# Kernel tuning notes

Measured on AMD Instinct MI355X. Metric: run time of the kernel, lower is better.

## Reference

```python
import jax, jax.numpy as jnp
import numpy as np

B, LAGS, POOL, D, H, NTS = 16, 4096, 4, 512, 8, 1000
S = LAGS // POOL          # num_pools = 1024
DH = D // H               # head dim = 64


def _layernorm_dim1(x, gamma, beta, eps=1e-5):
    # torch code: mean/var over dim=1 (channel axis), unbiased var, per-position affine
    mean = jnp.mean(x, axis=1, keepdims=True)
    var = jnp.var(x, axis=1, keepdims=True, ddof=1)
    unit = (x - mean) / jnp.sqrt(eps + var)
    return gamma * unit + beta


def setup_inputs() -> dict:
    key = jax.random.key(0)
    ks = jax.random.split(key, 16)
    inp = {
        "ts": jax.random.normal(ks[0], (B, 1, LAGS), dtype=jnp.float32),
        "te": jax.random.randint(ks[1], (B, 1), 0, NTS),
        "conv_w": jax.random.normal(ks[2], (D, 1, POOL), dtype=jnp.float32) * (1.0 / POOL) ** 0.5,
        "conv_b": jax.random.normal(ks[3], (D,), dtype=jnp.float32) * 0.02,
        "pe_emb": jax.random.normal(ks[4], (S, D), dtype=jnp.float32),
        "ts_emb": jax.random.normal(ks[5], (NTS, D), dtype=jnp.float32),
        "ln1_g": jnp.ones((S,), dtype=jnp.float32),
        "ln1_b": jnp.zeros((S,), dtype=jnp.float32),
        "dense_M": jax.random.normal(ks[6], (D, D), dtype=jnp.float32) * D ** -0.5,
        "Wq": jax.random.normal(ks[7], (H, DH, D), dtype=jnp.float32) * D ** -0.5,
        "Wk": jax.random.normal(ks[8], (H, DH, D), dtype=jnp.float32) * D ** -0.5,
        "Wv": jax.random.normal(ks[9], (H, DH, D), dtype=jnp.float32) * D ** -0.5,
        "Wo": jax.random.normal(ks[10], (D, D), dtype=jnp.float32) * D ** -0.5,
        "bo": jnp.zeros((D, 1), dtype=jnp.float32),
        "ln2_g": jnp.ones((S,), dtype=jnp.float32),
        "ln2_b": jnp.zeros((S,), dtype=jnp.float32),
    }
    return inp


def _forward(ts, te, conv_w, conv_b, pe_emb, ts_emb, ln1_g, ln1_b,
             dense_M, Wq, Wk, Wv, Wo, bo, ln2_g, ln2_b):
    # Conv1d with stride == kernel_size: non-overlapping patches
    xr = ts.reshape(B, S, POOL)                                   # (B,S,P)
    conv = jnp.einsum('bsp,dp->bds', xr, conv_w[:, 0, :]) + conv_b[:, None]  # (B,D,S)
    conv = conv + pe_emb.T                                        # positional add (D,S)
    act = jax.nn.gelu(conv, approximate=False)
    n1 = _layernorm_dim1(act, ln1_g, ln1_b)
    dense = jnp.einsum('ed,bds->bes', dense_M, n1)                # Linear: M @ x
    dense = dense + ts_emb[te[:, 0]][:, :, None]                  # ts embedding (B,D,1)

    # multi-head attention, Q=K=V=dense; vectorized over heads
    Qd = jnp.einsum('hcd,bds->bhcs', Wq, dense)                   # (B,H,DH,S)
    Kd = jnp.einsum('hcd,bds->bhcs', Wk, dense)
    Vd = jnp.einsum('hcd,bds->bhcs', Wv, dense)
    scores = jnp.einsum('bhci,bhcj->bhij', Qd, Kd) / DH ** 0.5    # (B,H,S,S)
    i_idx = jnp.arange(S)
    mask = i_idx[:, None] > i_idx[None, :]                        # tril(diagonal=-1): i>j -> -inf
    scores = jnp.where(mask, -jnp.inf, scores)
    sm = jax.nn.softmax(scores, axis=2)                           # softmax over dim 1 of (S,S)
    attn = jnp.einsum('bhci,bhij->bhcj', Vd, sm)                  # V @ softmaxed
    cat = attn.reshape(B, D, S)                                   # concat heads on dim 1
    out = jnp.einsum('ed,bds->bes', Wo, cat) + bo[None]           # final linear + bias
    res = out + conv                                              # residual
    return _layernorm_dim1(res, ln2_g, ln2_b)


def reference(ts, te, conv_w, conv_b, pe_emb, ts_emb, ln1_g, ln1_b,
              dense_M, Wq, Wk, Wv, Wo, bo, ln2_g, ln2_b):
    return _forward(ts, te, conv_w, conv_b, pe_emb, ts_emb, ln1_g, ln1_b,
                    dense_M, Wq, Wk, Wv, Wo, bo, ln2_g, ln2_b)
```

## Files before the change

### kernel.cpp

```cpp
#include <hip/hip_runtime.h>
#include <hip/hip_bf16.h>

#define B_ 16
#define S_ 1024
#define D_ 512
#define H_ 8
#define DH_ 64

typedef __attribute__((ext_vector_type(8))) short bf16x8;
typedef __attribute__((ext_vector_type(4))) short bf16x4;
typedef __attribute__((ext_vector_type(4))) float f32x4;
typedef __attribute__((ext_vector_type(16))) float f32x16;

__device__ __forceinline__ short f2bf(float f) {
    __hip_bfloat16 h = __float2bfloat16(f);
    return *reinterpret_cast<short*>(&h);
}
__device__ __forceinline__ unsigned pack_bf2(float lo, float hi) {
    unsigned a = (unsigned)(unsigned short)f2bf(lo);
    unsigned b = (unsigned)(unsigned short)f2bf(hi);
    return a | (b << 16);
}
__device__ __forceinline__ void gload16(const void* g, void* l) {
    __builtin_amdgcn_global_load_lds(
        (const __attribute__((address_space(1))) unsigned int*)g,
        (__attribute__((address_space(3))) unsigned int*)l, 16, 0, 0);
}

__global__ __launch_bounds__(256) void prep_w(
    const float* __restrict__ M, const float* __restrict__ Wq,
    const float* __restrict__ Wk, const float* __restrict__ Wv,
    const float* __restrict__ Wo, __hip_bfloat16* __restrict__ wb)
{
    __hip_bfloat16* wsrc = wb;
    __hip_bfloat16* Wob  = wb + 786432;
    __hip_bfloat16* MT   = wb + 1048576;

    const int gid = blockIdx.x * 256 + threadIdx.x;
    const int e8 = gid * 8;
    const int w = e8 >> 18;
    const int off = e8 & 262143;
    const float* src = (w == 0) ? M : (w == 1) ? Wq : (w == 2) ? Wk
                      : (w == 3) ? Wv : Wo;
    const float scale = (w == 1) ? 0.18033688011112042f : 1.0f;
    const float4 f0 = *reinterpret_cast<const float4*>(src + off);
    const float4 f1 = *reinterpret_cast<const float4*>(src + off + 4);
    float fv[8] = {f0.x, f0.y, f0.z, f0.w, f1.x, f1.y, f1.z, f1.w};

    if (w == 0) {
        const int e = off >> 9, d0 = off & 511;
#pragma unroll
        for (int j = 0; j < 8; ++j)
            MT[(size_t)(d0 + j) * 512 + e] = __float2bfloat16(fv[j]);
    } else {
        union { short s[8]; bf16x8 v; } r;
#pragma unroll
        for (int j = 0; j < 8; ++j) r.s[j] = f2bf(fv[j] * scale);
        __hip_bfloat16* dst = (w == 4) ? (Wob + off) : (wsrc + (w - 1) * 262144 + off);
        *reinterpret_cast<bf16x8*>(dst) = r.v;
    }
}

__global__ __launch_bounds__(256) void bias_k(
    const float* __restrict__ Wq, const float* __restrict__ Wk,
    const float* __restrict__ Wv, const float* __restrict__ ts_emb,
    const int* __restrict__ te, float* __restrict__ qkvbias)
{
    const int blk = blockIdx.x;
    const int w = blk >> 4, b = blk & 15;
    const float* W = (w == 0) ? Wq : (w == 1) ? Wk : Wv;
    const float scale = (w == 0) ? 0.18033688011112042f : 1.0f;
    const float* e = ts_emb + (size_t)te[b] * 512;
#pragma unroll
    for (int rep = 0; rep < 2; ++rep) {
        const int n = threadIdx.x + rep * 256;
        const float* wr = W + (size_t)n * 512;
        float s = 0.f;
        for (int d = 0; d < 512; d += 4) {
            const float4 a = *reinterpret_cast<const float4*>(wr + d);
            const float4 bb = *reinterpret_cast<const float4*>(e + d);
            s += a.x * bb.x + a.y * bb.y + a.z * bb.z + a.w * bb.w;
        }
        qkvbias[(size_t)(w * 16 + b) * 512 + n] = s * scale;
    }
}

__global__ __launch_bounds__(256) void k1_conv_gelu_ln(
    const float* __restrict__ ts, const float* __restrict__ conv_w,
    const float* __restrict__ conv_b, const float* __restrict__ pe,
    const float* __restrict__ g1, const float* __restrict__ b1,
    __hip_bfloat16* __restrict__ n1)
{
    const int w = threadIdx.x >> 6, lane = threadIdx.x & 63;
    const int row = blockIdx.x * 4 + w;
    const int b = row >> 10, s = row & 1023;
    const float4 x = *reinterpret_cast<const float4*>(ts + b * 4096 + s * 4);
    const int d0 = lane * 8;

    const float4 cb0 = *reinterpret_cast<const float4*>(conv_b + d0);
    const float4 cb1 = *reinterpret_cast<const float4*>(conv_b + d0 + 4);
    const float4 pe0 = *reinterpret_cast<const float4*>(pe + s * 512 + d0);
    const float4 pe1 = *reinterpret_cast<const float4*>(pe + s * 512 + d0 + 4);
    const float cbv[8] = {cb0.x, cb0.y, cb0.z, cb0.w, cb1.x, cb1.y, cb1.z, cb1.w};
    const float pev[8] = {pe0.x, pe0.y, pe0.z, pe0.w, pe1.x, pe1.y, pe1.z, pe1.w};

    float a[8];
    float sum = 0.f, sq = 0.f;
#pragma unroll
    for (int j = 0; j < 8; ++j) {
        const float4 wv = *reinterpret_cast<const float4*>(conv_w + (d0 + j) * 4);
        float v = x.x * wv.x + x.y * wv.y + x.z * wv.z + x.w * wv.w
                + cbv[j] + pev[j];
        v = 0.5f * v * (1.0f + erff(v * 0.70710678118654752f));
        a[j] = v; sum += v; sq += v * v;
    }
#pragma unroll
    for (int off = 1; off < 64; off <<= 1) {
        sum += __shfl_xor(sum, off);
        sq  += __shfl_xor(sq, off);
    }
    const float mean = sum * (1.0f / 512.0f);
    const float var  = (sq - 512.0f * mean * mean) * (1.0f / 511.0f);
    const float rstd = rsqrtf(var + 1e-5f);
    const float gg = g1[s], bb = b1[s];
    union { short sh[8]; bf16x8 v; } o;
#pragma unroll
    for (int j = 0; j < 8; ++j)
        o.sh[j] = f2bf(gg * ((a[j] - mean) * rstd) + bb);
    *reinterpret_cast<bf16x8*>(n1 + (size_t)row * 512 + d0) = o.v;
}

template<int MODE>
__global__ __launch_bounds__(256, 2) void gemm_k(
    const __hip_bfloat16* __restrict__ A,
    const __hip_bfloat16* __restrict__ Wb,
    void* __restrict__ outp,
    const float* __restrict__ aux)
{
    __shared__ char lA[2][128 * 128];
    __shared__ char lB[2][128 * 128];

    const int t = threadIdx.x;
    const int lane = t & 63;
    const int w = t >> 6;
    const int wm = w & 1, wn = w >> 1;
    const int Rb = blockIdx.x * 128;
    const int Nb = blockIdx.y * 128;
    const int g = lane >> 4, lr = lane & 15;
    const int lrow = lane >> 3;
    const int coff = ((lane & 7) ^ lrow) * 8;

    const __hip_bfloat16* asrc = A  + (size_t)(Rb + lrow) * 512 + coff;
    const __hip_bfloat16* bsrc = Wb + (size_t)(Nb + lrow) * 512 + coff;

    f32x4 acc[4][4];
#pragma unroll
    for (int i = 0; i < 4; ++i)
#pragma unroll
        for (int j = 0; j < 4; ++j) acc[i][j] = {0.f, 0.f, 0.f, 0.f};

    auto stage = [&](int buf, int k0) {
#pragma unroll
        for (int i = 0; i < 4; ++i) {
            const int r0 = w * 32 + i * 8;
            gload16(asrc + (size_t)r0 * 512 + k0, &lA[buf][r0 * 128]);
        }
#pragma unroll
        for (int i = 0; i < 4; ++i) {
            const int r0 = w * 32 + i * 8;
            gload16(bsrc + (size_t)r0 * 512 + k0, &lB[buf][r0 * 128]);
        }
    };

    stage(0, 0);
    __syncthreads();

    for (int kt = 0; kt < 8; ++kt) {
        const int buf = kt & 1;
        if (kt < 7) stage(buf ^ 1, (kt + 1) * 64);
#pragma unroll
        for (int kk = 0; kk < 2; ++kk) {
            bf16x8 af[4], bfv[4];
            const int ch = kk * 4 + g;
#pragma unroll
            for (int mt = 0; mt < 4; ++mt) {
                const int row = wm * 64 + mt * 16 + lr;
                af[mt] = *reinterpret_cast<const bf16x8*>(
                    &lA[buf][row * 128 + ((ch ^ (row & 7)) << 4)]);
            }
#pragma unroll
            for (int nt = 0; nt < 4; ++nt) {
                const int row = wn * 64 + nt * 16 + lr;
                bfv[nt] = *reinterpret_cast<const bf16x8*>(
                    &lB[buf][row * 128 + ((ch ^ (row & 7)) << 4)]);
            }
#pragma unroll
            for (int mt = 0; mt < 4; ++mt)
#pragma unroll
                for (int nt = 0; nt < 4; ++nt)
                    acc[mt][nt] = __builtin_amdgcn_mfma_f32_16x16x32_bf16(
                        af[mt], bfv[nt], acc[mt][nt], 0, 0, 0);
        }
        __syncthreads();
    }

    const int w3 = Nb >> 9;
#pragma unroll
    for (int mt = 0; mt < 4; ++mt) {
#pragma unroll
        for (int nt = 0; nt < 4; ++nt) {
#pragma unroll
            for (int r = 0; r < 4; ++r) {
                const int R = Rb + wm * 64 + mt * 16 + 4 * g + r;
                const int N = Nb + wn * 64 + nt * 16 + lr;
                float v = acc[mt][nt][r];
                if (MODE == 5) {
                    const int Nl = N & 511;
                    const int b = R >> 10, s = R & 1023, h = Nl >> 6, c = Nl & 63;
                    v += aux[(size_t)(w3 * 16 + b) * 512 + Nl];
                    __hip_bfloat16* base =
                        reinterpret_cast<__hip_bfloat16*>(outp) + (size_t)w3 * 8388608;
                    if (w3 == 2)
                        base[(((size_t)(b * 8 + h)) * 64 + c) * 1024 + s] =
                            __float2bfloat16(v);
                    else
                        base[(((size_t)(b * 8 + h)) * 1024 + s) * 64 + c] =
                            __float2bfloat16(v);
                } else if (MODE == 6) {
                    reinterpret_cast<__hip_bfloat16*>(outp)[(size_t)R * 512 + N] =
                        __float2bfloat16(v);
                } else {
                    reinterpret_cast<float*>(outp)[(size_t)R * 512 + N] = v + aux[N];
                }
            }
        }
    }
}

__device__ __forceinline__ void write_strip(
    __hip_bfloat16* __restrict__ dstbase, const int jw0,
    const f32x16& o0, const f32x16& o1, const float lsum,
    const int l5, const int ln31)
{
    const float linv = 1.0f / lsum;
#pragma unroll
    for (int r = 0; r < 16; ++r) {
        const int jrow = (r & 3) + 8 * (r >> 2) + 4 * l5;
        const float rinv = __shfl(linv, jrow);
        __hip_bfloat16* dst = dstbase + (size_t)(jw0 + jrow) * 512;
        dst[ln31]      = __float2bfloat16(o0[r] * rinv);
        dst[32 + ln31] = __float2bfloat16(o1[r] * rinv);
    }
}

__global__ __launch_bounds__(256, 4) void attn5_k(
    const __hip_bfloat16* __restrict__ Qm,
    const __hip_bfloat16* __restrict__ Km,
    const __hip_bfloat16* __restrict__ Vt,
    __hip_bfloat16* __restrict__ cat)
{
    __shared__ char qbuf[2][4096];
    __shared__ char vbuf[2][4096];

    const int t = threadIdx.x, lane = t & 63, w = t >> 6;
    const int l5 = lane >> 5, ln31 = lane & 31;
    const int id = blockIdx.x;
    const int bh = id & 127;
    const int jb = (0x32451067u >> ((id >> 7) * 4)) & 7;
    const int b = bh >> 3, h = bh & 7;
    const int j0 = jb * 128 + w * 32;

    const __hip_bfloat16* Qh = Qm + (size_t)bh * (S_ * 64);
    const __hip_bfloat16* Kh = Km + (size_t)bh * (S_ * 64);
    const __hip_bfloat16* Vh = Vt + (size_t)bh * (64 * S_);

    bf16x8 kf[4];
#pragma unroll
    for (int kt = 0; kt < 4; ++kt)
        kf[kt] = *reinterpret_cast<const bf16x8*>(
            Kh + (size_t)(j0 + ln31) * 64 + kt * 16 + l5 * 8);

    f32x16 o0, o1;
#pragma unroll
    for (int r = 0; r < 16; ++r) { o0[r] = 0.f; o1[r] = 0.f; }
    float m = -3e38f, lsum = 0.f;

    const int last = jb * 4 + w;
    const int ntiles = jb * 4 + 4;

    const int q_row  = w * 8 + (lane >> 3);
    const int q_ch   = (lane & 7) ^ (lane >> 3);
    const int v_row  = w * 16 + (lane >> 2);
    const int v_ch   = (lane & 3) ^ ((lane >> 2) & 3) ^ ((lane >> 4) & 3);
    const __hip_bfloat16* qsrc = Qh + (size_t)q_row * 64 + q_ch * 8;
    const __hip_bfloat16* vsrc = Vh + (size_t)v_row * 1024 + v_ch * 8;

    auto stage = [&](int buf, int tile) {
        const int i0 = tile * 32;
        gload16(qsrc + (size_t)i0 * 64, &qbuf[buf][w * 1024]);
        gload16(vsrc + i0,              &vbuf[buf][w * 1024]);
    };

    stage(0, 0);
    __syncthreads();

    for (int tt = 0; tt < ntiles; ++tt) {
        const int buf = tt & 1;
        if (tt + 1 < ntiles) stage(buf ^ 1, tt + 1);
        if (tt <= last) {
            f32x16 sc;
#pragma unroll
            for (int r = 0; r < 16; ++r) sc[r] = 0.f;
            bf16x8 qf[4];
#pragma unroll
            for (int kt = 0; kt < 4; ++kt)
                qf[kt] = *reinterpret_cast<const bf16x8*>(
                    &qbuf[buf][ln31 * 128 + (((kt * 2 + l5) ^ (ln31 & 7)) << 4)]);
#pragma unroll
            for (int kt = 0; kt < 4; ++kt)
                sc = __builtin_amdgcn_mfma_f32_32x32x16_bf16(qf[kt], kf[kt], sc, 0, 0, 0);

            union u8 { bf16x4 h[2]; bf16x8 v; };
            u8 vf[2][2];
#pragma unroll
            for (int kt = 0; kt < 2; ++kt) {
#pragma unroll
                for (int dh = 0; dh < 2; ++dh) {
                    const int drow = ln31 + dh * 32;
                    const int swz = (drow & 3) ^ ((drow >> 2) & 3);
                    const int x0 = kt * 32 + 8 * l5;
#pragma unroll
                    for (int hp = 0; hp < 2; ++hp) {
                        const int x = x0 + hp * 16;
                        vf[kt][dh].h[hp] = *reinterpret_cast<const bf16x4*>(
                            &vbuf[buf][drow * 64 + (((x >> 4) ^ swz) << 4) + (x & 15)]);
                    }
                }
            }

            const bool diag = (tt == last);
            float p[16];
            float mx = -3e38f;
            if (diag) {
#pragma unroll
                for (int r = 0; r < 16; ++r) {
                    const int irow = (r & 3) + 8 * (r >> 2) + 4 * l5;
                    const float v = (irow > ln31) ? -3e38f : sc[r];
                    p[r] = v; mx = fmaxf(mx, v);
                }
            } else {
#pragma unroll
                for (int r = 0; r < 16; ++r) { p[r] = sc[r]; mx = fmaxf(mx, sc[r]); }
            }
            mx = fmaxf(mx, __shfl_xor(mx, 32));
            if (!__all(mx <= m + 8.0f)) {
                const float mn = fmaxf(m, mx);
                const float alpha = exp2f(m - mn);
                m = mn; lsum *= alpha;
#pragma unroll
                for (int r = 0; r < 16; ++r) {
                    const int jrow = (r & 3) + 8 * (r >> 2) + 4 * l5;
                    const float ar = __shfl(alpha, jrow);
                    o0[r] *= ar; o1[r] *= ar;
                }
            }
            float ps = 0.f;
#pragma unroll
            for (int r = 0; r < 16; ++r) { p[r] = exp2f(p[r] - m); ps += p[r]; }
            ps += __shfl_xor(ps, 32);
            lsum += ps;

            union { unsigned u[4]; bf16x8 v; } pa0, pa1;
            pa0.u[0] = pack_bf2(p[0],  p[1]);  pa0.u[1] = pack_bf2(p[2],  p[3]);
            pa0.u[2] = pack_bf2(p[4],  p[5]);  pa0.u[3] = pack_bf2(p[6],  p[7]);
            pa1.u[0] = pack_bf2(p[8],  p[9]);  pa1.u[1] = pack_bf2(p[10], p[11]);
            pa1.u[2] = pack_bf2(p[12], p[13]); pa1.u[3] = pack_bf2(p[14], p[15]);
            o0 = __builtin_amdgcn_mfma_f32_32x32x16_bf16(pa0.v, vf[0][0].v, o0, 0, 0, 0);
            o1 = __builtin_amdgcn_mfma_f32_32x32x16_bf16(pa0.v, vf[0][1].v, o1, 0, 0, 0);
            o0 = __builtin_amdgcn_mfma_f32_32x32x16_bf16(pa1.v, vf[1][0].v, o0, 0, 0, 0);
            o1 = __builtin_amdgcn_mfma_f32_32x32x16_bf16(pa1.v, vf[1][1].v, o1, 0, 0, 0);
        }
        __syncthreads();
    }

    __hip_bfloat16* dstbase = cat + (size_t)b * 1024 * 512 + h * 64;
    write_strip(dstbase, j0, o0, o1, lsum, l5, ln31);
}

__global__ __launch_bounds__(256) void k5_res_ln(
    const float* __restrict__ outf,
    const float* __restrict__ ts, const float* __restrict__ conv_w,
    const float* __restrict__ conv_b, const float* __restrict__ pe,
    const float* __restrict__ g2, const float* __restrict__ b2,
    float* __restrict__ out)
{
    __shared__ float tile[16 * 520];
    const int blk = blockIdx.x;
    const int b = blk >> 6, s0 = (blk & 63) * 16;
    const int t = threadIdx.x;
    const int sl = t >> 4, c = t & 15;
    const int s = s0 + sl;

    const float4 x = *reinterpret_cast<const float4*>(ts + b * 4096 + s * 4);
    float vals[32];
    float sum = 0.f, sq = 0.f;
#pragma unroll
    for (int j = 0; j < 32; ++j) {
        const int d = c + 16 * j;
        const float4 wv = *reinterpret_cast<const float4*>(conv_w + d * 4);
        const float conv = x.x * wv.x + x.y * wv.y + x.z * wv.z + x.w * wv.w
                         + conv_b[d] + pe[s * 512 + d];
        const float a = outf[(size_t)(b * 1024 + s) * 512 + d] + conv;
        vals[j] = a; sum += a; sq += a * a;
    }
#pragma unroll
    for (int off = 1; off < 16; off <<= 1) {
        sum += __shfl_xor(sum, off);
        sq  += __shfl_xor(sq, off);
    }
    const float mean = sum * (1.0f / 512.0f);
    const float var  = (sq - 512.0f * mean * mean) * (1.0f / 511.0f);
    const float rstd = rsqrtf(var + 1e-5f);
    const float gg = g2[s], bb = b2[s];
#pragma unroll
    for (int j = 0; j < 32; ++j) {
        const int d = c + 16 * j;
        tile[sl * 520 + d] = gg * ((vals[j] - mean) * rstd) + bb;
    }
    __syncthreads();
#pragma unroll
    for (int q2 = 0; q2 < 2; ++q2) {
        const int d = t + q2 * 256;
        float buf[16];
#pragma unroll
        for (int sl2 = 0; sl2 < 16; ++sl2) buf[sl2] = tile[sl2 * 520 + d];
        float4* dst = reinterpret_cast<float4*>(
            out + ((size_t)b * 512 + d) * 1024 + s0);
        dst[0] = make_float4(buf[0],  buf[1],  buf[2],  buf[3]);
        dst[1] = make_float4(buf[4],  buf[5],  buf[6],  buf[7]);
        dst[2] = make_float4(buf[8],  buf[9],  buf[10], buf[11]);
        dst[3] = make_float4(buf[12], buf[13], buf[14], buf[15]);
    }
}

extern "C" void kernel_launch(void* const* d_in, const int* in_sizes, int n_in,
                              void* d_out, int out_size, void* d_ws, size_t ws_size,
                              hipStream_t stream)
{
    const float* ts     = (const float*)d_in[0];
    const int*   te     = (const int*)d_in[1];
    const float* conv_w = (const float*)d_in[2];
    const float* conv_b = (const float*)d_in[3];
    const float* pe     = (const float*)d_in[4];
    const float* ts_emb = (const float*)d_in[5];
    const float* g1     = (const float*)d_in[6];
    const float* b1     = (const float*)d_in[7];
    const float* M      = (const float*)d_in[8];
    const float* Wq     = (const float*)d_in[9];
    const float* Wk     = (const float*)d_in[10];
    const float* Wv     = (const float*)d_in[11];
    const float* Wo     = (const float*)d_in[12];
    const float* bo     = (const float*)d_in[13];
    const float* g2     = (const float*)d_in[14];
    const float* b2     = (const float*)d_in[15];

    char* ws = (char*)d_ws;
    __hip_bfloat16* wb     = (__hip_bfloat16*)(ws);
    __hip_bfloat16* wsrc   = wb;
    __hip_bfloat16* Wob    = wb + 786432;
    __hip_bfloat16* MT     = wb + 1048576;
    __hip_bfloat16* Wqkvp  = (__hip_bfloat16*)(ws + (2688ull << 10));
    float*          qkvbias= (float*)(ws + (4608ull << 10));
    __hip_bfloat16* n1     = (__hip_bfloat16*)(ws + ( 6ull << 20));
    __hip_bfloat16* cat    = n1;
    __hip_bfloat16* q      = (__hip_bfloat16*)(ws + (22ull << 20));
    __hip_bfloat16* k      = (__hip_bfloat16*)(ws + (38ull << 20));
    __hip_bfloat16* vT     = (__hip_bfloat16*)(ws + (54ull << 20));
    float*          outf   = (float*)(ws + (22ull << 20));

    prep_w<<<640, 256, 0, stream>>>(M, Wq, Wk, Wv, Wo, wb);
    bias_k<<<48, 256, 0, stream>>>(Wq, Wk, Wv, ts_emb, te, qkvbias);
    gemm_k<6><<<dim3(12, 4), 256, 0, stream>>>(wsrc, MT, Wqkvp, nullptr);
    k1_conv_gelu_ln<<<4096, 256, 0, stream>>>(ts, conv_w, conv_b, pe, g1, b1, n1);
    gemm_k<5><<<dim3(128, 12), 256, 0, stream>>>(n1, Wqkvp, q, qkvbias);
    attn5_k<<<1024, 256, 0, stream>>>(q, k, vT, cat);
    gemm_k<3><<<dim3(128, 4), 256, 0, stream>>>(cat, Wob, outf, bo);
    k5_res_ln<<<1024, 256, 0, stream>>>(outf, ts, conv_w, conv_b, pe, g2, b2,
                                        (float*)d_out);
}
```

Baseline: 198.1 us.

## Transpose M via LDS tiles and split bias dot products across blocks

prep_w now transposes the dense matrix through a 32x33 shared-memory tile, so the MT writes are coalesced instead of strided scalar stores. bias_k now reads the bf16 prescaled weights and splits each 512-long dot product into four 128-element chunks across 4x more blocks, writing partial sums. The QKV GEMM epilogue adds the four partials together. This raises parallelism in small prep kernels, at the cost of extra epilogue loads and of using bf16-rounded weights in the bias, which slightly changes precision.

```diff
diff --git a/kernel.cpp b/kernel.cpp
--- a/kernel.cpp
+++ b/kernel.cpp
@@ -16,6 +16,10 @@
     __hip_bfloat16 h = __float2bfloat16(f);
     return *reinterpret_cast<short*>(&h);
 }
+__device__ __forceinline__ float bf2f(short s) {
+    unsigned u = ((unsigned)(unsigned short)s) << 16;
+    return __uint_as_float(u);
+}
 __device__ __forceinline__ unsigned pack_bf2(float lo, float hi) {
     unsigned a = (unsigned)(unsigned short)f2bf(lo);
     unsigned b = (unsigned)(unsigned short)f2bf(hi);
@@ -36,52 +40,60 @@
     __hip_bfloat16* Wob  = wb + 786432;
     __hip_bfloat16* MT   = wb + 1048576;
 
-    const int gid = blockIdx.x * 256 + threadIdx.x;
-    const int e8 = gid * 8;
-    const int w = e8 >> 18;
-    const int off = e8 & 262143;
-    const float* src = (w == 0) ? M : (w == 1) ? Wq : (w == 2) ? Wk
-                      : (w == 3) ? Wv : Wo;
-    const float scale = (w == 1) ? 0.18033688011112042f : 1.0f;
-    const float4 f0 = *reinterpret_cast<const float4*>(src + off);
-    const float4 f1 = *reinterpret_cast<const float4*>(src + off + 4);
-    float fv[8] = {f0.x, f0.y, f0.z, f0.w, f1.x, f1.y, f1.z, f1.w};
-
-    if (w == 0) {
-        const int e = off >> 9, d0 = off & 511;
-#pragma unroll
-        for (int j = 0; j < 8; ++j)
-            MT[(size_t)(d0 + j) * 512 + e] = __float2bfloat16(fv[j]);
+    const int blk = blockIdx.x, t = threadIdx.x;
+    if (blk < 512) {
+        const int wi = blk >> 7;
+        const int off = (blk & 127) * 2048 + t * 8;
+        const float* src = (wi == 0) ? Wq : (wi == 1) ? Wk : (wi == 2) ? Wv : Wo;
+        const float scale = (wi == 0) ? 0.18033688011112042f : 1.0f;
+        const float4 f0 = *reinterpret_cast<const float4*>(src + off);
+        const float4 f1 = *reinterpret_cast<const float4*>(src + off + 4);
+        const float fv[8] = {f0.x, f0.y, f0.z, f0.w, f1.x, f1.y, f1.z, f1.w};
+        union { short s[8]; bf16x8 v; } r;
+#pragma unroll
+        for (int j = 0; j < 8; ++j) r.s[j] = f2bf(fv[j] * scale);
+        __hip_bfloat16* dst = (wi == 3) ? (Wob + off) : (wsrc + wi * 262144 + off);
+        *reinterpret_cast<bf16x8*>(dst) = r.v;
     } else {
-        union { short s[8]; bf16x8 v; } r;
-#pragma unroll
-        for (int j = 0; j < 8; ++j) r.s[j] = f2bf(fv[j] * scale);
-        __hip_bfloat16* dst = (w == 4) ? (Wob + off) : (wsrc + (w - 1) * 262144 + off);
-        *reinterpret_cast<bf16x8*>(dst) = r.v;
+        __shared__ float tile[32][33];
+        const int tt = blk - 512;
+        const int e0 = (tt & 15) * 32, d0 = (tt >> 4) * 32;
+        const int r = t >> 5, c = t & 31;
+#pragma unroll
+        for (int k = 0; k < 4; ++k)
+            tile[r + k * 8][c] = M[(size_t)(e0 + r + k * 8) * 512 + d0 + c];
+        __syncthreads();
+#pragma unroll
+        for (int k = 0; k < 4; ++k)
+            MT[(size_t)(d0 + r + k * 8) * 512 + e0 + c] =
+                __float2bfloat16(tile[c][r + k * 8]);
     }
 }
 
 __global__ __launch_bounds__(256) void bias_k(
-    const float* __restrict__ Wq, const float* __restrict__ Wk,
-    const float* __restrict__ Wv, const float* __restrict__ ts_emb,
-    const int* __restrict__ te, float* __restrict__ qkvbias)
+    const __hip_bfloat16* __restrict__ wsrc, const float* __restrict__ ts_emb,
+    const int* __restrict__ te, float* __restrict__ qkvpart)
 {
     const int blk = blockIdx.x;
-    const int w = blk >> 4, b = blk & 15;
-    const float* W = (w == 0) ? Wq : (w == 1) ? Wk : Wv;
-    const float scale = (w == 0) ? 0.18033688011112042f : 1.0f;
-    const float* e = ts_emb + (size_t)te[b] * 512;
+    const int w16b = blk >> 2, dc = blk & 3;
+    const int b = w16b & 15, w = w16b >> 4;
+    const float* e = ts_emb + (size_t)te[b] * 512 + dc * 128;
 #pragma unroll
     for (int rep = 0; rep < 2; ++rep) {
         const int n = threadIdx.x + rep * 256;
-        const float* wr = W + (size_t)n * 512;
+        const __hip_bfloat16* wr = wsrc + ((size_t)(w * 512 + n)) * 512 + dc * 128;
         float s = 0.f;
-        for (int d = 0; d < 512; d += 4) {
-            const float4 a = *reinterpret_cast<const float4*>(wr + d);
-            const float4 bb = *reinterpret_cast<const float4*>(e + d);
-            s += a.x * bb.x + a.y * bb.y + a.z * bb.z + a.w * bb.w;
+#pragma unroll 4
+        for (int d8 = 0; d8 < 128; d8 += 8) {
+            const bf16x8 wv8 = *reinterpret_cast<const bf16x8*>(wr + d8);
+            const float4 e0 = *reinterpret_cast<const float4*>(e + d8);
+            const float4 e1 = *reinterpret_cast<const float4*>(e + d8 + 4);
+            s += bf2f(wv8[0]) * e0.x + bf2f(wv8[1]) * e0.y
+               + bf2f(wv8[2]) * e0.z + bf2f(wv8[3]) * e0.w
+               + bf2f(wv8[4]) * e1.x + bf2f(wv8[5]) * e1.y
+               + bf2f(wv8[6]) * e1.z + bf2f(wv8[7]) * e1.w;
         }
-        qkvbias[(size_t)(w * 16 + b) * 512 + n] = s * scale;
+        qkvpart[(size_t)dc * 24576 + (size_t)w16b * 512 + n] = s;
     }
 }
 
@@ -217,7 +229,8 @@
                 if (MODE == 5) {
                     const int Nl = N & 511;
                     const int b = R >> 10, s = R & 1023, h = Nl >> 6, c = Nl & 63;
-                    v += aux[(size_t)(w3 * 16 + b) * 512 + Nl];
+                    const float* qp = aux + (size_t)(w3 * 16 + b) * 512 + Nl;
+                    v += qp[0] + qp[24576] + qp[49152] + qp[73728];
                     __hip_bfloat16* base =
                         reinterpret_cast<__hip_bfloat16*>(outp) + (size_t)w3 * 8388608;
                     if (w3 == 2)
@@ -470,7 +483,7 @@
     __hip_bfloat16* Wob    = wb + 786432;
     __hip_bfloat16* MT     = wb + 1048576;
     __hip_bfloat16* Wqkvp  = (__hip_bfloat16*)(ws + (2688ull << 10));
-    float*          qkvbias= (float*)(ws + (4608ull << 10));
+    float*          qkvpart= (float*)(ws + (4608ull << 10));
     __hip_bfloat16* n1     = (__hip_bfloat16*)(ws + ( 6ull << 20));
     __hip_bfloat16* cat    = n1;
     __hip_bfloat16* q      = (__hip_bfloat16*)(ws + (22ull << 20));
@@ -478,11 +491,11 @@
     __hip_bfloat16* vT     = (__hip_bfloat16*)(ws + (54ull << 20));
     float*          outf   = (float*)(ws + (22ull << 20));
 
-    prep_w<<<640, 256, 0, stream>>>(M, Wq, Wk, Wv, Wo, wb);
-    bias_k<<<48, 256, 0, stream>>>(Wq, Wk, Wv, ts_emb, te, qkvbias);
+    prep_w<<<768, 256, 0, stream>>>(M, Wq, Wk, Wv, Wo, wb);
+    bias_k<<<192, 256, 0, stream>>>(wsrc, ts_emb, te, qkvpart);
     gemm_k<6><<<dim3(12, 4), 256, 0, stream>>>(wsrc, MT, Wqkvp, nullptr);
     k1_conv_gelu_ln<<<4096, 256, 0, stream>>>(ts, conv_w, conv_b, pe, g1, b1, n1);
-    gemm_k<5><<<dim3(128, 12), 256, 0, stream>>>(n1, Wqkvp, q, qkvbias);
+    gemm_k<5><<<dim3(128, 12), 256, 0, stream>>>(n1, Wqkvp, q, qkvpart);
     attn5_k<<<1024, 256, 0, stream>>>(q, k, vT, cat);
     gemm_k<3><<<dim3(128, 4), 256, 0, stream>>>(cat, Wob, outf, bo);
     k5_res_ln<<<1024, 256, 0, stream>>>(outf, ts, conv_w, conv_b, pe, g2, b2,
```

After: 174.3 us. -12.1%, faster.
